# Kernel optimization log

Hardware: AMD Instinct MI355X
Metric: run time of the kernel (lower is better)

## Reference

```python
import jax, jax.numpy as jnp
import numpy as np

N_NODES = 40000
N_EDGES = 640000
IN_DIM = 128
HID_DIM = 128


def _glorot(key, shape):
    fan_in, fan_out = shape[1], shape[0]
    lim = np.sqrt(6.0 / (fan_in + fan_out))
    return jax.random.uniform(key, shape, jnp.float32, -lim, lim)


def setup_inputs() -> dict:
    key = jax.random.key(0)
    ks = jax.random.split(key, 8)
    x = jax.random.normal(ks[0], (N_NODES, IN_DIM), dtype=jnp.float32)
    edge_index = jax.random.randint(ks[1], (2, N_EDGES), 0, N_NODES, dtype=jnp.int64)
    # SAGEConv params: lin_l (applied to aggregated neighbors, has bias), lin_r (self, no bias)
    W1l = _glorot(ks[2], (HID_DIM, IN_DIM))
    b1l = jnp.zeros((HID_DIM,), jnp.float32)
    W1r = _glorot(ks[3], (HID_DIM, IN_DIM))
    W2l = _glorot(ks[4], (HID_DIM, HID_DIM))
    b2l = jnp.zeros((HID_DIM,), jnp.float32)
    W2r = _glorot(ks[5], (HID_DIM, HID_DIM))
    return {"x": x, "edge_index": edge_index, "W1l": W1l, "b1l": b1l,
            "W1r": W1r, "W2l": W2l, "b2l": b2l, "W2r": W2r}


def _sage_conv(x, src, dst, Wl, bl, Wr):
    # mean aggregation of source features into destination nodes
    msg = x[src]  # [E, D] gather
    agg = jax.ops.segment_sum(msg, dst, num_segments=N_NODES)          # [N, D]
    cnt = jax.ops.segment_sum(jnp.ones_like(dst, jnp.float32), dst,
                              num_segments=N_NODES)                     # [N]
    mean = agg / jnp.maximum(cnt, 1.0)[:, None]
    # out = lin_l(mean_neighbors) + lin_r(x)
    return mean @ Wl.T + bl + x @ Wr.T


def reference(x, edge_index, W1l, b1l, W1r, W2l, b2l, W2r):
    src, dst = edge_index[0], edge_index[1]
    h = jax.nn.relu(_sage_conv(x, src, dst, W1l, b1l, W1r))
    h = jax.nn.relu(_sage_conv(h, src, dst, W2l, b2l, W2r))
    return h
```

## Files before the change

### kernel.cpp

```cpp
#include <hip/hip_runtime.h>
#include <hip/hip_bf16.h>

#define DIM 128
#define NN 40000
#define NE 640000
#define NBLK ((NN + 255) / 256)

typedef __attribute__((ext_vector_type(8))) short s16x8;
typedef __attribute__((ext_vector_type(4))) float f32x4;
typedef __attribute__((ext_vector_type(4))) unsigned short u16x4;
typedef __attribute__((ext_vector_type(4))) unsigned int u32x4;

__device__ __forceinline__ float bf16_lo(unsigned v) { return __uint_as_float(v << 16); }
__device__ __forceinline__ float bf16_hi(unsigned v) { return __uint_as_float(v & 0xffff0000u); }
__device__ __forceinline__ unsigned short f_to_bf16(float f) {
    unsigned u = __float_as_uint(f);
    u += 0x7fffu + ((u >> 16) & 1u);
    return (unsigned short)(u >> 16);
}

__global__ void fill_const_f32(float* __restrict__ out, int n, float v) {
    int i = blockIdx.x * blockDim.x + threadIdx.x;
    if (i < n) out[i] = v;
}

__global__ void cvt_all(const float* __restrict__ x, unsigned short* __restrict__ xb,
                        const float* __restrict__ w0, const float* __restrict__ w1,
                        const float* __restrict__ w2, const float* __restrict__ w3,
                        unsigned short* __restrict__ wb,
                        int* __restrict__ deg, const int* __restrict__ ei,
                        int* __restrict__ flag) {
    int b = blockIdx.x;
    if (b >= 5064) {
        int i = (b - 5064) * 256 + threadIdx.x;
        if (i < NN) deg[i] = 0;
        if (b == 5064 && threadIdx.x < 64) {
            int w = ei[2 * threadIdx.x + 1];
            unsigned long long m = __ballot(w == 0);
            if (threadIdx.x == 0) *flag = (m == ~0ull) ? 1 : 0;
        }
        return;
    }
    const float* src;
    unsigned short* dst;
    size_t i;
    if (b < 5000) {
        src = x; dst = xb;
        i = (size_t)b * 256 + threadIdx.x;
    } else {
        int w = b - 5000;
        int m = w >> 4;
        src = (m == 0) ? w0 : (m == 1) ? w1 : (m == 2) ? w2 : w3;
        dst = wb + (size_t)m * 16384;
        i = (size_t)(w & 15) * 256 + threadIdx.x;
    }
    f32x4 v = *(const f32x4*)(src + 4 * i);
    u16x4 o;
    o.x = f_to_bf16(v.x); o.y = f_to_bf16(v.y);
    o.z = f_to_bf16(v.z); o.w = f_to_bf16(v.w);
    *(u16x4*)(dst + 4 * i) = o;
}


__global__ void count_deg(const int* __restrict__ ei, const int* __restrict__ fmt,
                          int* __restrict__ deg) {
    int e = blockIdx.x * blockDim.x + threadIdx.x;
    if (e >= NE) return;
    int dst = (*fmt) ? ((const int2*)ei)[NE + e].x : ei[NE + e];
    if ((unsigned)dst < (unsigned)NN) atomicAdd(&deg[dst], 1);
}

__global__ void block_sums(const int* __restrict__ deg, int* __restrict__ bsum) {
    __shared__ int sh[256];
    int i = blockIdx.x * 256 + threadIdx.x;
    sh[threadIdx.x] = (i < NN) ? deg[i] : 0;
    __syncthreads();
    for (int off = 128; off > 0; off >>= 1) {
        if (threadIdx.x < off) sh[threadIdx.x] += sh[threadIdx.x + off];
        __syncthreads();
    }
    if (threadIdx.x == 0) bsum[blockIdx.x] = sh[0];
}

__global__ void scan_block2(const int* __restrict__ deg, const int* __restrict__ bsum,
                            int* __restrict__ row_ptr, int* __restrict__ cursor) {
    __shared__ int sh[256];
    int t = threadIdx.x, bid = blockIdx.x;

    int v0 = (t < NBLK) ? bsum[t] : 0;
    sh[t] = v0;
    __syncthreads();
    for (int off = 1; off < 256; off <<= 1) {
        int u = (t >= off) ? sh[t - off] : 0;
        __syncthreads();
        sh[t] += u;
        __syncthreads();
    }
    int base = sh[bid] - bsum[bid];
    __syncthreads();

    int i = bid * 256 + t;
    int v = (i < NN) ? deg[i] : 0;
    sh[t] = v;
    __syncthreads();
    for (int off = 1; off < 256; off <<= 1) {
        int u = (t >= off) ? sh[t - off] : 0;
        __syncthreads();
        sh[t] += u;
        __syncthreads();
    }
    int excl = sh[t] - v + base;
    if (i < NN) { row_ptr[i] = excl; cursor[i] = excl; }
    if (i == NN - 1) row_ptr[NN] = excl + v;
}

__global__ void fill_csr(const int* __restrict__ ei, const int* __restrict__ fmt,
                         int* __restrict__ cursor, int* __restrict__ sorted_src) {
    int e = blockIdx.x * blockDim.x + threadIdx.x;
    if (e >= NE) return;
    int src, dst;
    if (*fmt) {
        src = ((const int2*)ei)[e].x;
        dst = ((const int2*)ei)[NE + e].x;
    } else {
        src = ei[e];
        dst = ei[NE + e];
    }
    if ((unsigned)dst >= (unsigned)NN) return;
    int pos = atomicAdd(&cursor[dst], 1);
    if ((unsigned)pos < (unsigned)NE) sorted_src[pos] = src;
}


#define ACC8(A, v)                                 \
    A[0] += bf16_lo((v).x); A[1] += bf16_hi((v).x); \
    A[2] += bf16_lo((v).y); A[3] += bf16_hi((v).y); \
    A[4] += bf16_lo((v).z); A[5] += bf16_hi((v).z); \
    A[6] += bf16_lo((v).w); A[7] += bf16_hi((v).w);

template <bool WRITE_F32>
__global__ __launch_bounds__(512) void sage_layer(
    const unsigned short* __restrict__ xin,
    const int* __restrict__ row_ptr,
    const int* __restrict__ sorted_src,
    const unsigned short* __restrict__ Wl,
    const unsigned short* __restrict__ Wr,
    const float* __restrict__ bias,
    void* __restrict__ outv) {
    __shared__ unsigned short lds_mean[64 * 128];
    __shared__ unsigned short lds_hs[64 * 128];

    int tid = threadIdx.x;
    int lane = tid & 63;
    int wv = tid >> 6;
    int row0 = blockIdx.x * 64;

    {
        int r = tid >> 3;
        int lid0 = (tid & 7) * 2;
        int lid1 = lid0 + 1;
        const unsigned short* src = xin + (size_t)(row0 + r) * DIM + lid0 * 8;
        u32x4 v0 = *(const u32x4*)(src);
        u32x4 v1 = *(const u32x4*)(src + 8);
        int base = (r >> 4) * 2048;
        int o0 = base + (lid0 >> 2) * 512 + (lid0 & 3) * 128 + (((r & 15) ^ lid0) * 8);
        int o1 = base + (lid1 >> 2) * 512 + (lid1 & 3) * 128 + (((r & 15) ^ lid1) * 8);
        *(u32x4*)(lds_hs + o0) = v0;
        *(u32x4*)(lds_hs + o1) = v1;
    }

    {
        int grp = lane >> 4;
        int lid = lane & 15;
        int gbase = grp << 4;
        int g = wv * 4 + grp;
        for (int it = 0; it < 2; ++it) {
            int nb = it * 32 + g;
            int n = row0 + nb;
            int start = row_ptr[n], end = row_ptr[n + 1];

            float a[8] = {0.f, 0.f, 0.f, 0.f, 0.f, 0.f, 0.f, 0.f};
            float b[8] = {0.f, 0.f, 0.f, 0.f, 0.f, 0.f, 0.f, 0.f};

            int i = start;
            for (; i + 16 <= end; i += 16) {
                int idx = sorted_src[i + lid];
#pragma unroll
                for (int j = 0; j < 16; j += 4) {
                    int s0 = __shfl(idx, gbase + j);
                    int s1 = __shfl(idx, gbase + j + 1);
                    int s2 = __shfl(idx, gbase + j + 2);
                    int s3 = __shfl(idx, gbase + j + 3);
                    u32x4 v0 = *(const u32x4*)(xin + (size_t)s0 * DIM + lid * 8);
                    u32x4 v1 = *(const u32x4*)(xin + (size_t)s1 * DIM + lid * 8);
                    u32x4 v2 = *(const u32x4*)(xin + (size_t)s2 * DIM + lid * 8);
                    u32x4 v3 = *(const u32x4*)(xin + (size_t)s3 * DIM + lid * 8);
                    ACC8(a, v0);
                    ACC8(b, v1);
                    ACC8(a, v2);
                    ACC8(b, v3);
                }
            }
            int rem = end - i;
            if (rem > 0) {
                int src_i = (i + lid < end) ? (i + lid) : (end - 1);
                int idx = sorted_src[src_i];
#pragma unroll
                for (int j = 0; j < 16; ++j) {
                    if (j < rem) {
                        int s = __shfl(idx, gbase + j);
                        u32x4 v = *(const u32x4*)(xin + (size_t)s * DIM + lid * 8);
                        if (j & 1) { ACC8(b, v); }
                        else       { ACC8(a, v); }
                    }
                }
            }
#pragma unroll
            for (int k = 0; k < 8; ++k) a[k] += b[k];

            int d = end - start;
            float inv = 1.f / (float)(d > 1 ? d : 1);
            u32x4 o;
            o.x = (unsigned)f_to_bf16(a[0] * inv) | ((unsigned)f_to_bf16(a[1] * inv) << 16);
            o.y = (unsigned)f_to_bf16(a[2] * inv) | ((unsigned)f_to_bf16(a[3] * inv) << 16);
            o.z = (unsigned)f_to_bf16(a[4] * inv) | ((unsigned)f_to_bf16(a[5] * inv) << 16);
            o.w = (unsigned)f_to_bf16(a[6] * inv) | ((unsigned)f_to_bf16(a[7] * inv) << 16);
            int off = (nb >> 4) * 2048 + (lid >> 2) * 512 + (lid & 3) * 128
                    + (((nb & 15) ^ lid) * 8);
            *(u32x4*)(lds_mean + off) = o;
        }
    }

    __syncthreads();

    {
        int quad = lane >> 4;
        int m16 = lane & 15;
        int bcol = wv * 16 + m16;
        const unsigned short* wl0 = Wl + (size_t)bcol * DIM + quad * 8;
        const unsigned short* wr0 = Wr + (size_t)bcol * DIM + quad * 8;
        s16x8 bl[4], br[4];
#pragma unroll
        for (int kb = 0; kb < 4; ++kb) {
            bl[kb] = *(const s16x8*)(wl0 + kb * 32);
            br[kb] = *(const s16x8*)(wr0 + kb * 32);
        }
        f32x4 acc[4] = {{0,0,0,0},{0,0,0,0},{0,0,0,0},{0,0,0,0}};
#pragma unroll
        for (int t = 0; t < 4; ++t) {
#pragma unroll
            for (int kb = 0; kb < 4; ++kb) {
                int lo = (lane ^ ((kb << 2) | quad)) << 3;
                s16x8 am = *(const s16x8*)(lds_mean + t * 2048 + kb * 512 + lo);
                acc[t] = __builtin_amdgcn_mfma_f32_16x16x32_bf16(am, bl[kb], acc[t], 0, 0, 0);
            }
#pragma unroll
            for (int kb = 0; kb < 4; ++kb) {
                int lo = (lane ^ ((kb << 2) | quad)) << 3;
                s16x8 ah = *(const s16x8*)(lds_hs + t * 2048 + kb * 512 + lo);
                acc[t] = __builtin_amdgcn_mfma_f32_16x16x32_bf16(ah, br[kb], acc[t], 0, 0, 0);
            }
        }
        float bv = bias[bcol];
#pragma unroll
        for (int t = 0; t < 4; ++t) {
#pragma unroll
            for (int r = 0; r < 4; ++r) {
                int orow = row0 + t * 16 + quad * 4 + r;
                float v = fmaxf(acc[t][r] + bv, 0.f);
                if (WRITE_F32)
                    ((float*)outv)[(size_t)orow * DIM + bcol] = v;
                else
                    ((unsigned short*)outv)[(size_t)orow * DIM + bcol] = f_to_bf16(v);
            }
        }
    }
}


extern "C" void kernel_launch(void* const* d_in, const int* in_sizes, int n_in,
                              void* d_out, int out_size, void* d_ws, size_t ws_size,
                              hipStream_t stream) {
    const float* x   = (const float*)d_in[0];
    const int*   ei  = (const int*)d_in[1];
    const float* W1l = (const float*)d_in[2];
    const float* b1l = (const float*)d_in[3];
    const float* W1r = (const float*)d_in[4];
    const float* W2l = (const float*)d_in[5];
    const float* b2l = (const float*)d_in[6];
    const float* W2r = (const float*)d_in[7];
    float* out = (float*)d_out;

    const int OUT_ELEMS = NN * DIM;

    const size_t OFF_DEG  = 0;
    const size_t OFF_ROW  = 163840;
    const size_t OFF_BSUM = 324608;
    const size_t OFF_CUR  = 327680;
    const size_t OFF_FMT  = 491264;
    const size_t OFF_SRT  = 491520;
    const size_t OFF_WB   = 3051520;
    const size_t OFF_XB   = 3182592;
    const size_t OFF_H1   = 23662592;
    const size_t NEEDED   = 33902592;

    if (ws_size < NEEDED) {
        fill_const_f32<<<(OUT_ELEMS + 255) / 256, 256, 0, stream>>>(out, OUT_ELEMS, 50.0f);
        return;
    }

    char* ws = (char*)d_ws;
    int* deg     = (int*)(ws + OFF_DEG);
    int* row_ptr = (int*)(ws + OFF_ROW);
    int* bsum    = (int*)(ws + OFF_BSUM);
    int* cursor  = (int*)(ws + OFF_CUR);
    int* fmtflag = (int*)(ws + OFF_FMT);
    int* sorted  = (int*)(ws + OFF_SRT);
    unsigned short* Wb    = (unsigned short*)(ws + OFF_WB);
    unsigned short* xb    = (unsigned short*)(ws + OFF_XB);
    unsigned short* h1b   = (unsigned short*)(ws + OFF_H1);
    unsigned short* W1lb = Wb;
    unsigned short* W1rb = Wb + 16384;
    unsigned short* W2lb = Wb + 32768;
    unsigned short* W2rb = Wb + 49152;

    cvt_all<<<5221, 256, 0, stream>>>(x, xb, W1l, W1r, W2l, W2r, Wb, deg, ei, fmtflag);
    count_deg<<<(NE + 255) / 256, 256, 0, stream>>>(ei, fmtflag, deg);
    block_sums<<<NBLK, 256, 0, stream>>>(deg, bsum);
    scan_block2<<<NBLK, 256, 0, stream>>>(deg, bsum, row_ptr, cursor);
    fill_csr<<<(NE + 255) / 256, 256, 0, stream>>>(ei, fmtflag, cursor, sorted);

    sage_layer<false><<<NN / 64, 512, 0, stream>>>(xb, row_ptr, sorted, W1lb, W1rb, b1l, h1b);
    sage_layer<true><<<NN / 64, 512, 0, stream>>>(h1b, row_ptr, sorted, W2lb, W2rb, b2l, out);
}
```

Baseline: 229.9 us.

## Fuse degree counting into conversion kernel and software-pipeline neighbor gathers

Merges degree counting into the conversion kernel, with deg zeroed by a memset instead of in-kernel writes. fill_csr now handles four edges per thread to batch its loads. The aggregation loop in sage_layer is restructured to preload up to 48 neighbor indices per node and double-buffer eight-wide gathers, using masked FMA weights in place of branches. The aim is fewer launches and more memory-level parallelism in the gather, at the cost of higher register pressure and wasted loads for low-degree nodes.

```diff
diff --git a/kernel.cpp b/kernel.cpp
--- a/kernel.cpp
+++ b/kernel.cpp
@@ -30,14 +30,21 @@
                         unsigned short* __restrict__ wb,
                         int* __restrict__ deg, const int* __restrict__ ei,
                         int* __restrict__ flag) {
+    __shared__ int sfmt;
     int b = blockIdx.x;
     if (b >= 5064) {
-        int i = (b - 5064) * 256 + threadIdx.x;
-        if (i < NN) deg[i] = 0;
-        if (b == 5064 && threadIdx.x < 64) {
+        if (threadIdx.x < 64) {
             int w = ei[2 * threadIdx.x + 1];
             unsigned long long m = __ballot(w == 0);
-            if (threadIdx.x == 0) *flag = (m == ~0ull) ? 1 : 0;
+            if (threadIdx.x == 0) sfmt = (m == ~0ull) ? 1 : 0;
+        }
+        __syncthreads();
+        int f = sfmt;
+        if (b == 5064 && threadIdx.x == 0) *flag = f;
+        int e = (b - 5064) * 256 + threadIdx.x;
+        if (e < NE) {
+            int dst = f ? ((const int2*)ei)[NE + e].x : ei[NE + e];
+            if ((unsigned)dst < (unsigned)NN) atomicAdd(&deg[dst], 1);
         }
         return;
     }
@@ -62,14 +69,6 @@
 }
 
 
-__global__ void count_deg(const int* __restrict__ ei, const int* __restrict__ fmt,
-                          int* __restrict__ deg) {
-    int e = blockIdx.x * blockDim.x + threadIdx.x;
-    if (e >= NE) return;
-    int dst = (*fmt) ? ((const int2*)ei)[NE + e].x : ei[NE + e];
-    if ((unsigned)dst < (unsigned)NN) atomicAdd(&deg[dst], 1);
-}
-
 __global__ void block_sums(const int* __restrict__ deg, int* __restrict__ bsum) {
     __shared__ int sh[256];
     int i = blockIdx.x * 256 + threadIdx.x;
@@ -116,27 +115,112 @@
 
 __global__ void fill_csr(const int* __restrict__ ei, const int* __restrict__ fmt,
                          int* __restrict__ cursor, int* __restrict__ sorted_src) {
-    int e = blockIdx.x * blockDim.x + threadIdx.x;
-    if (e >= NE) return;
-    int src, dst;
-    if (*fmt) {
-        src = ((const int2*)ei)[e].x;
-        dst = ((const int2*)ei)[NE + e].x;
-    } else {
-        src = ei[e];
-        dst = ei[NE + e];
-    }
-    if ((unsigned)dst >= (unsigned)NN) return;
-    int pos = atomicAdd(&cursor[dst], 1);
-    if ((unsigned)pos < (unsigned)NE) sorted_src[pos] = src;
-}
-
-
-#define ACC8(A, v)                                 \
-    A[0] += bf16_lo((v).x); A[1] += bf16_hi((v).x); \
-    A[2] += bf16_lo((v).y); A[3] += bf16_hi((v).y); \
-    A[4] += bf16_lo((v).z); A[5] += bf16_hi((v).z); \
-    A[6] += bf16_lo((v).w); A[7] += bf16_hi((v).w);
+    int gid = blockIdx.x * blockDim.x + threadIdx.x;
+    int f = *fmt;
+    int s[4], dd[4];
+#pragma unroll
+    for (int u = 0; u < 4; ++u) {
+        int e = gid + u * 160000;
+        if (f) {
+            s[u]  = ((const int2*)ei)[e].x;
+            dd[u] = ((const int2*)ei)[NE + e].x;
+        } else {
+            s[u]  = ei[e];
+            dd[u] = ei[NE + e];
+        }
+    }
+#pragma unroll
+    for (int u = 0; u < 4; ++u) {
+        if ((unsigned)dd[u] < (unsigned)NN) {
+            int pos = atomicAdd(&cursor[dd[u]], 1);
+            if ((unsigned)pos < (unsigned)NE) sorted_src[pos] = s[u];
+        }
+    }
+}
+
+
+#define ACC8W(A, v, W)                                         \
+    A[0] = fmaf(W, bf16_lo((v).x), A[0]);                      \
+    A[1] = fmaf(W, bf16_hi((v).x), A[1]);                      \
+    A[2] = fmaf(W, bf16_lo((v).y), A[2]);                      \
+    A[3] = fmaf(W, bf16_hi((v).y), A[3]);                      \
+    A[4] = fmaf(W, bf16_lo((v).z), A[4]);                      \
+    A[5] = fmaf(W, bf16_hi((v).z), A[5]);                      \
+    A[6] = fmaf(W, bf16_lo((v).w), A[6]);                      \
+    A[7] = fmaf(W, bf16_hi((v).w), A[7]);
+
+#define GL1(DST, EE, D, DM1, I0, I1, I2)                               \
+    {                                                                   \
+        int ce_ = ((EE) < (D)) ? (EE) : (DM1);                          \
+        int ix_ = (ce_ >= 32) ? (I2) : ((ce_ >= 16) ? (I1) : (I0));     \
+        int s_ = __shfl(ix_, gbase + (ce_ & 15));                       \
+        DST = *(const u32x4*)(xin + (size_t)s_ * DIM + lid * 8);        \
+    }
+
+#define GLOAD8(B, E0, D, DM1, I0, I1, I2)        \
+    GL1(B[0], (E0) + 0, D, DM1, I0, I1, I2)      \
+    GL1(B[1], (E0) + 1, D, DM1, I0, I1, I2)      \
+    GL1(B[2], (E0) + 2, D, DM1, I0, I1, I2)      \
+    GL1(B[3], (E0) + 3, D, DM1, I0, I1, I2)      \
+    GL1(B[4], (E0) + 4, D, DM1, I0, I1, I2)      \
+    GL1(B[5], (E0) + 5, D, DM1, I0, I1, I2)      \
+    GL1(B[6], (E0) + 6, D, DM1, I0, I1, I2)      \
+    GL1(B[7], (E0) + 7, D, DM1, I0, I1, I2)
+
+#define GA1(AA, BK, EE, D)                                  \
+    { float wt_ = ((EE) < (D)) ? 1.f : 0.f; ACC8W(AA, BK, wt_); }
+
+#define GACC8(AA, BB, B, E0, D)       \
+    GA1(AA, B[0], (E0) + 0, D)        \
+    GA1(BB, B[1], (E0) + 1, D)        \
+    GA1(AA, B[2], (E0) + 2, D)        \
+    GA1(BB, B[3], (E0) + 3, D)        \
+    GA1(AA, B[4], (E0) + 4, D)        \
+    GA1(BB, B[5], (E0) + 5, D)        \
+    GA1(AA, B[6], (E0) + 6, D)        \
+    GA1(BB, B[7], (E0) + 7, D)
+
+#define GLT1(DST, K)                                                    \
+    {   int cj_ = ((K) < rem_) ? (K) : rm1_;                            \
+        int s_ = __shfl(idx_, gbase + cj_);                             \
+        DST = *(const u32x4*)(xin + (size_t)s_ * DIM + lid * 8); }
+#define GAT1(AA, BK, K)                                                 \
+    {   float wt_ = ((K) < rem_) ? 1.f : 0.f; ACC8W(AA, BK, wt_); }
+
+#define NODE_STREAM(AA, BB, ST, EN, D, I0, I1, I2)                       \
+    if ((D) > 0) {                                                        \
+        int dm1_ = (D) - 1;                                               \
+        int ds_ = ((D) < 48) ? (D) : 48;                                  \
+        GLOAD8(U_, 0, D, dm1_, I0, I1, I2)                                \
+        if (ds_ > 8)  { GLOAD8(V_, 8, D, dm1_, I0, I1, I2) }              \
+        GACC8(AA, BB, U_, 0, D)                                           \
+        if (ds_ > 16) { GLOAD8(U_, 16, D, dm1_, I0, I1, I2) }             \
+        if (ds_ > 8)  { GACC8(AA, BB, V_, 8, D) }                         \
+        if (ds_ > 24) { GLOAD8(V_, 24, D, dm1_, I0, I1, I2) }             \
+        if (ds_ > 16) { GACC8(AA, BB, U_, 16, D) }                        \
+        if (ds_ > 32) { GLOAD8(U_, 32, D, dm1_, I0, I1, I2) }             \
+        if (ds_ > 24) { GACC8(AA, BB, V_, 24, D) }                        \
+        if (ds_ > 40) { GLOAD8(V_, 40, D, dm1_, I0, I1, I2) }             \
+        if (ds_ > 32) { GACC8(AA, BB, U_, 32, D) }                        \
+        if (ds_ > 40) { GACC8(AA, BB, V_, 40, D) }                        \
+        for (int ii_ = (ST) + 48; ii_ < (EN); ii_ += 16) {                \
+            int rem_ = (EN) - ii_;  if (rem_ > 16) rem_ = 16;             \
+            int rm1_ = rem_ - 1;                                          \
+            int idx_ = sorted_src[ii_ + ((lid < rem_) ? lid : rm1_)];     \
+            GLT1(U_[0], 0) GLT1(U_[1], 1) GLT1(U_[2], 2) GLT1(U_[3], 3)   \
+            GLT1(U_[4], 4) GLT1(U_[5], 5) GLT1(U_[6], 6) GLT1(U_[7], 7)   \
+            GLT1(V_[0], 8) GLT1(V_[1], 9) GLT1(V_[2],10) GLT1(V_[3],11)   \
+            GLT1(V_[4],12) GLT1(V_[5],13) GLT1(V_[6],14) GLT1(V_[7],15)   \
+            GAT1(AA, U_[0], 0) GAT1(BB, U_[1], 1)                         \
+            GAT1(AA, U_[2], 2) GAT1(BB, U_[3], 3)                         \
+            GAT1(AA, U_[4], 4) GAT1(BB, U_[5], 5)                         \
+            GAT1(AA, U_[6], 6) GAT1(BB, U_[7], 7)                         \
+            GAT1(AA, V_[0], 8) GAT1(BB, V_[1], 9)                         \
+            GAT1(AA, V_[2],10) GAT1(BB, V_[3],11)                         \
+            GAT1(AA, V_[4],12) GAT1(BB, V_[5],13)                         \
+            GAT1(AA, V_[6],14) GAT1(BB, V_[7],15)                         \
+        }                                                                 \
+    }
 
 template <bool WRITE_F32>
 __global__ __launch_bounds__(512) void sage_layer(
@@ -174,57 +258,56 @@
         int lid = lane & 15;
         int gbase = grp << 4;
         int g = wv * 4 + grp;
-        for (int it = 0; it < 2; ++it) {
-            int nb = it * 32 + g;
-            int n = row0 + nb;
-            int start = row_ptr[n], end = row_ptr[n + 1];
-
-            float a[8] = {0.f, 0.f, 0.f, 0.f, 0.f, 0.f, 0.f, 0.f};
-            float b[8] = {0.f, 0.f, 0.f, 0.f, 0.f, 0.f, 0.f, 0.f};
-
-            int i = start;
-            for (; i + 16 <= end; i += 16) {
-                int idx = sorted_src[i + lid];
-#pragma unroll
-                for (int j = 0; j < 16; j += 4) {
-                    int s0 = __shfl(idx, gbase + j);
-                    int s1 = __shfl(idx, gbase + j + 1);
-                    int s2 = __shfl(idx, gbase + j + 2);
-                    int s3 = __shfl(idx, gbase + j + 3);
-                    u32x4 v0 = *(const u32x4*)(xin + (size_t)s0 * DIM + lid * 8);
-                    u32x4 v1 = *(const u32x4*)(xin + (size_t)s1 * DIM + lid * 8);
-                    u32x4 v2 = *(const u32x4*)(xin + (size_t)s2 * DIM + lid * 8);
-                    u32x4 v3 = *(const u32x4*)(xin + (size_t)s3 * DIM + lid * 8);
-                    ACC8(a, v0);
-                    ACC8(b, v1);
-                    ACC8(a, v2);
-                    ACC8(b, v3);
-                }
-            }
-            int rem = end - i;
-            if (rem > 0) {
-                int src_i = (i + lid < end) ? (i + lid) : (end - 1);
-                int idx = sorted_src[src_i];
-#pragma unroll
-                for (int j = 0; j < 16; ++j) {
-                    if (j < rem) {
-                        int s = __shfl(idx, gbase + j);
-                        u32x4 v = *(const u32x4*)(xin + (size_t)s * DIM + lid * 8);
-                        if (j & 1) { ACC8(b, v); }
-                        else       { ACC8(a, v); }
-                    }
-                }
-            }
-#pragma unroll
-            for (int k = 0; k < 8; ++k) a[k] += b[k];
-
-            int d = end - start;
-            float inv = 1.f / (float)(d > 1 ? d : 1);
+
+        int n0 = row0 + g, n1 = row0 + 32 + g;
+        int st0 = row_ptr[n0], en0 = row_ptr[n0 + 1];
+        int st1 = row_ptr[n1], en1 = row_ptr[n1 + 1];
+        int d0 = en0 - st0, d1 = en1 - st1;
+
+        int i0 = 0, i1 = 0, i2 = 0, j0 = 0, j1 = 0, j2 = 0;
+        if (d0 > 0) {
+            int dm = d0 - 1;
+            i0 = sorted_src[st0 + ((lid      < d0) ? lid      : dm)];
+            i1 = sorted_src[st0 + ((16 + lid < d0) ? 16 + lid : dm)];
+            i2 = sorted_src[st0 + ((32 + lid < d0) ? 32 + lid : dm)];
+        }
+        if (d1 > 0) {
+            int dm = d1 - 1;
+            j0 = sorted_src[st1 + ((lid      < d1) ? lid      : dm)];
+            j1 = sorted_src[st1 + ((16 + lid < d1) ? 16 + lid : dm)];
+            j2 = sorted_src[st1 + ((32 + lid < d1) ? 32 + lid : dm)];
+        }
+
+        u32x4 U_[8], V_[8];
+        float a[8] = {0.f, 0.f, 0.f, 0.f, 0.f, 0.f, 0.f, 0.f};
+        float b[8] = {0.f, 0.f, 0.f, 0.f, 0.f, 0.f, 0.f, 0.f};
+
+        NODE_STREAM(a, b, st0, en0, d0, i0, i1, i2)
+        {
+            float inv = 1.f / (float)(d0 > 1 ? d0 : 1);
             u32x4 o;
-            o.x = (unsigned)f_to_bf16(a[0] * inv) | ((unsigned)f_to_bf16(a[1] * inv) << 16);
-            o.y = (unsigned)f_to_bf16(a[2] * inv) | ((unsigned)f_to_bf16(a[3] * inv) << 16);
-            o.z = (unsigned)f_to_bf16(a[4] * inv) | ((unsigned)f_to_bf16(a[5] * inv) << 16);
-            o.w = (unsigned)f_to_bf16(a[6] * inv) | ((unsigned)f_to_bf16(a[7] * inv) << 16);
+            o.x = (unsigned)f_to_bf16((a[0] + b[0]) * inv) | ((unsigned)f_to_bf16((a[1] + b[1]) * inv) << 16);
+            o.y = (unsigned)f_to_bf16((a[2] + b[2]) * inv) | ((unsigned)f_to_bf16((a[3] + b[3]) * inv) << 16);
+            o.z = (unsigned)f_to_bf16((a[4] + b[4]) * inv) | ((unsigned)f_to_bf16((a[5] + b[5]) * inv) << 16);
+            o.w = (unsigned)f_to_bf16((a[6] + b[6]) * inv) | ((unsigned)f_to_bf16((a[7] + b[7]) * inv) << 16);
+            int nb = g;
+            int off = (nb >> 4) * 2048 + (lid >> 2) * 512 + (lid & 3) * 128
+                    + (((nb & 15) ^ lid) * 8);
+            *(u32x4*)(lds_mean + off) = o;
+        }
+
+#pragma unroll
+        for (int k = 0; k < 8; ++k) { a[k] = 0.f; b[k] = 0.f; }
+
+        NODE_STREAM(a, b, st1, en1, d1, j0, j1, j2)
+        {
+            float inv = 1.f / (float)(d1 > 1 ? d1 : 1);
+            u32x4 o;
+            o.x = (unsigned)f_to_bf16((a[0] + b[0]) * inv) | ((unsigned)f_to_bf16((a[1] + b[1]) * inv) << 16);
+            o.y = (unsigned)f_to_bf16((a[2] + b[2]) * inv) | ((unsigned)f_to_bf16((a[3] + b[3]) * inv) << 16);
+            o.z = (unsigned)f_to_bf16((a[4] + b[4]) * inv) | ((unsigned)f_to_bf16((a[5] + b[5]) * inv) << 16);
+            o.w = (unsigned)f_to_bf16((a[6] + b[6]) * inv) | ((unsigned)f_to_bf16((a[7] + b[7]) * inv) << 16);
+            int nb = 32 + g;
             int off = (nb >> 4) * 2048 + (lid >> 2) * 512 + (lid & 3) * 128
                     + (((nb & 15) ^ lid) * 8);
             *(u32x4*)(lds_mean + off) = o;
@@ -324,11 +407,11 @@
     unsigned short* W2lb = Wb + 32768;
     unsigned short* W2rb = Wb + 49152;
 
-    cvt_all<<<5221, 256, 0, stream>>>(x, xb, W1l, W1r, W2l, W2r, Wb, deg, ei, fmtflag);
-    count_deg<<<(NE + 255) / 256, 256, 0, stream>>>(ei, fmtflag, deg);
+    hipMemsetAsync(deg, 0, NN * sizeof(int), stream);
+    cvt_all<<<7564, 256, 0, stream>>>(x, xb, W1l, W1r, W2l, W2r, Wb, deg, ei, fmtflag);
     block_sums<<<NBLK, 256, 0, stream>>>(deg, bsum);
     scan_block2<<<NBLK, 256, 0, stream>>>(deg, bsum, row_ptr, cursor);
-    fill_csr<<<(NE + 255) / 256, 256, 0, stream>>>(ei, fmtflag, cursor, sorted);
+    fill_csr<<<625, 256, 0, stream>>>(ei, fmtflag, cursor, sorted);
 
     sage_layer<false><<<NN / 64, 512, 0, stream>>>(xb, row_ptr, sorted, W1lb, W1rb, b1l, h1b);
     sage_layer<true><<<NN / 64, 512, 0, stream>>>(h1b, row_ptr, sorted, W2lb, W2rb, b2l, out);
```

After: 223.1 us. 3.0% less time.
